# Kernel optimization log

Measured on AMD Instinct MI355X. Metric: run time of the kernel, lower is better.

The kernel has to match this reference:

```python
import jax, jax.numpy as jnp
import numpy as np
from jax import lax

K = 10
ALPHA = 0.1
N_NODES = 100000
N_EDGES = 3200000


def setup_inputs() -> dict:
    key = jax.random.key(0)
    ks = jax.random.split(key, 6)
    x = jax.random.normal(ks[0], (N_NODES, 256), dtype=jnp.float32)
    edge_index = jax.random.randint(ks[1], (2, N_EDGES), 0, N_NODES, dtype=jnp.int64)
    w1 = jax.random.normal(ks[2], (256, 256), dtype=jnp.float32) * (1.0 / np.sqrt(256))
    b1 = jax.random.normal(ks[3], (256,), dtype=jnp.float32) * 0.01
    w2 = jax.random.normal(ks[4], (64, 256), dtype=jnp.float32) * (1.0 / np.sqrt(256))
    b2 = jax.random.normal(ks[5], (64,), dtype=jnp.float32) * 0.01
    return {"x": x, "edge_index": edge_index, "w1": w1, "b1": b1, "w2": w2, "b2": b2}


def reference(x, edge_index, w1, b1, w2, b2):
    # Eval mode: dropout is identity.
    h = jax.nn.relu(x @ w1.T + b1)          # [N, hidden]
    z = h @ w2.T + b2                        # [N, out]

    n = x.shape[0]
    loop = jnp.arange(n, dtype=edge_index.dtype)
    row = jnp.concatenate([edge_index[0], loop])   # sources (with self-loops)
    col = jnp.concatenate([edge_index[1], loop])   # targets (with self-loops)

    # gcn_norm: D^{-1/2} (A + I) D^{-1/2}, degree at target nodes
    deg = jax.ops.segment_sum(jnp.ones_like(col, dtype=z.dtype), col, num_segments=n)
    dinv = lax.rsqrt(deg)                    # deg >= 1 due to self-loops
    norm = dinv[row] * dinv[col]             # [E+N]

    x0 = z

    def step(xk, _):
        msg = xk[row] * norm[:, None]                          # gather + scale
        agg = jax.ops.segment_sum(msg, col, num_segments=n)    # scatter-add
        return (1.0 - ALPHA) * agg + ALPHA * x0, None

    out, _ = lax.scan(step, z, None, length=K)
    return out
```

## Files before the change

kernel.cpp:

```cpp
#include <hip/hip_runtime.h>
#include <hip/hip_bf16.h>


#define HIDDEN 256
#define OUTF   64
#define NB_BLK 256

typedef __attribute__((ext_vector_type(8))) unsigned short ushort8;
typedef __attribute__((ext_vector_type(8))) short short8v;
typedef __attribute__((ext_vector_type(4))) float f32x4;

__device__ inline float b2f(unsigned short u) {
    union { unsigned int i; float f; } c;
    c.i = ((unsigned int)u) << 16;
    return c.f;
}
__device__ inline unsigned short f2b(float f) {
    union { float f; unsigned int i; } c;
    c.f = f;
    unsigned int x = c.i;
    unsigned int r = (x + 0x7fff + ((x >> 16) & 1)) >> 16;
    return (unsigned short)r;
}
__device__ inline short8v cvt8v(float4 A, float4 B) {
    short8v o;
    o[0] = (short)f2b(A.x); o[1] = (short)f2b(A.y);
    o[2] = (short)f2b(A.z); o[3] = (short)f2b(A.w);
    o[4] = (short)f2b(B.x); o[5] = (short)f2b(B.y);
    o[6] = (short)f2b(B.z); o[7] = (short)f2b(B.w);
    return o;
}
__device__ inline short8v cvt8(const float* s) {
    return cvt8v(((const float4*)s)[0], ((const float4*)s)[1]);
}

__device__ inline bool detect_i64(const int* __restrict__ p) {
    int acc = 0;
#pragma unroll
    for (int i = 0; i < 16; ++i) acc |= p[2 * i + 1];
    return acc == 0;
}
__device__ inline int load_idx(const void* eiv, long long flat, bool is64) {
    if (is64) return (int)((const long long*)eiv)[flat];
    return ((const int*)eiv)[flat];
}

__global__ __launch_bounds__(256) void part_hist_kernel(const void* __restrict__ eiv,
                                                        long long E, int* __restrict__ bh,
                                                        int n, int nb) {
    __shared__ int hist[512];
    bool is64 = detect_i64((const int*)eiv);
    int t = threadIdx.x, b = blockIdx.x;
    for (int i = t; i < 512; i += 256) hist[i] = 0;
    __syncthreads();
    long long chunk = (E + NB_BLK - 1) / NB_BLK;
    long long beg = (long long)b * chunk, end = min(E, beg + chunk);
    for (long long e = beg + t; e < end; e += 256) {
        int c = load_idx(eiv, E + e, is64);
        if ((unsigned)c < (unsigned)n) atomicAdd(&hist[c >> 8], 1);
    }
    __syncthreads();
    for (int i = t; i < nb; i += 256) bh[i * NB_BLK + b] = hist[i];
}

__global__ __launch_bounds__(256) void part_colscan_kernel(const int* __restrict__ bh,
                                                           int* __restrict__ pre,
                                                           int* __restrict__ btot) {
    __shared__ int s[NB_BLK];
    int g = blockIdx.x, t = threadIdx.x;
    int v = bh[g * NB_BLK + t];
    s[t] = v;
    __syncthreads();
    for (int o = 1; o < NB_BLK; o <<= 1) {
        int tv = (t >= o) ? s[t - o] : 0;
        __syncthreads();
        s[t] += tv;
        __syncthreads();
    }
    pre[g * NB_BLK + t] = s[t] - v;
    if (t == NB_BLK - 1) btot[g] = s[t];
}

__global__ __launch_bounds__(512) void part_bscan_kernel(const int* __restrict__ btot,
                                                         int* __restrict__ bofs, int nb) {
    __shared__ int s[512];
    int t = threadIdx.x;
    int v = (t < nb) ? btot[t] : 0;
    s[t] = v;
    __syncthreads();
    for (int o = 1; o < 512; o <<= 1) {
        int tv = (t >= o) ? s[t - o] : 0;
        __syncthreads();
        s[t] += tv;
        __syncthreads();
    }
    if (t < nb) bofs[t] = s[t] - v;
    if (t == 511) bofs[nb] = s[511];
}

__global__ __launch_bounds__(256) void part_scatter_kernel(const void* __restrict__ eiv,
                                                           long long E,
                                                           const int* __restrict__ bofs,
                                                           const int* __restrict__ pre,
                                                           int2* __restrict__ pairs,
                                                           int n, int nb) {
    __shared__ int cur[512];
    bool is64 = detect_i64((const int*)eiv);
    int t = threadIdx.x, b = blockIdx.x;
    for (int i = t; i < nb; i += 256) cur[i] = bofs[i] + pre[i * NB_BLK + b];
    __syncthreads();
    long long chunk = (E + NB_BLK - 1) / NB_BLK;
    long long beg = (long long)b * chunk, end = min(E, beg + chunk);
    for (long long e = beg + t; e < end; e += 256) {
        int r = load_idx(eiv, e, is64);
        int c = load_idx(eiv, E + e, is64);
        if ((unsigned)c >= (unsigned)n || (unsigned)r >= (unsigned)n) continue;
        int pos = atomicAdd(&cur[c >> 8], 1);
        pairs[pos] = make_int2(c, r);
    }
}

__global__ __launch_bounds__(256) void csr_bucket_kernel(const int2* __restrict__ pairs,
                                                         const int* __restrict__ bofs,
                                                         int* __restrict__ ofs,
                                                         float* __restrict__ dinv,
                                                         int* __restrict__ csr_src,
                                                         int n, int nb) {
    __shared__ int hist[256];
    __shared__ int scn[256];
    int b = blockIdx.x;
    int t = threadIdx.x;
    int node0 = b << 8;
    int cnt = min(256, n - node0);

    hist[t] = 0;
    __syncthreads();
    int beg = bofs[b], end = bofs[b + 1];
    for (int e = beg + t; e < end; e += 256) atomicAdd(&hist[pairs[e].x & 255], 1);
    __syncthreads();
    int v = hist[t];
    scn[t] = v;
    __syncthreads();
    for (int o = 1; o < 256; o <<= 1) {
        int tv = (t >= o) ? scn[t - o] : 0;
        __syncthreads();
        scn[t] += tv;
        __syncthreads();
    }
    int excl = scn[t] - v;
    if (t < cnt) {
        ofs[node0 + t] = beg + excl;
        dinv[node0 + t] = rsqrtf((float)(v + 1));
    }
    if (b == nb - 1 && t == 0) ofs[n] = end;
    __syncthreads();
    hist[t] = beg + excl;
    __syncthreads();
    for (int e = beg + t; e < end; e += 256) {
        int2 p = pairs[e];
        int pos = atomicAdd(&hist[p.x & 255], 1);
        csr_src[pos] = p.y;
    }
}

__global__ __launch_bounds__(256) void pack_w_kernel(const float* __restrict__ w1,
                                                     const float* __restrict__ w2,
                                                     unsigned short* __restrict__ w1p,
                                                     unsigned short* __restrict__ w2p) {
    int id = blockIdx.x * 256 + threadIdx.x;
    if (id < 8192) {
        int ks = id >> 10, rem = id & 1023;
        int f = rem >> 2, kg = rem & 3;
        short8v o = cvt8(w1 + (size_t)f * HIDDEN + ks * 32 + kg * 8);
        *(short8v*)(w1p + ((size_t)(ks * 1024 + (f >> 4) * 64 + kg * 16 + (f & 15)) << 3)) = o;
    } else if (id < 8192 + 2048) {
        int q = id - 8192;
        int j = q >> 5, kslot = q & 31;
        short8v o = cvt8(w2 + (size_t)j * HIDDEN + kslot * 8);
        *(short8v*)(w2p +
                    ((size_t)((j >> 4) * 512 + (kslot >> 2) * 64 + (kslot & 3) * 16 + (j & 15))
                     << 3)) = o;
    }
}

__global__ __launch_bounds__(512) void mlp_mfma_kernel(const float* __restrict__ x,
                                                       const unsigned short* __restrict__ w1p,
                                                       const float* __restrict__ b1,
                                                       const unsigned short* __restrict__ w2p,
                                                       const float* __restrict__ b2,
                                                       const float* __restrict__ dinv,
                                                       unsigned short* __restrict__ xb0,
                                                       unsigned short* __restrict__ g0, int n) {
    __shared__ __align__(16) union {
        struct { unsigned short w1s[8192]; unsigned short xs[2048]; } p1;
        unsigned short h[64 * 264];
    } u;

    const int t = threadIdx.x;
    const int w = t >> 6;
    const int l = t & 63;
    const int c = l & 15, g = l >> 4;
    const int node0 = blockIdx.x * 64;

    const bool xrole = (t < 256);
    const int sm = t >> 2, skg = t & 3;
    const int snode = node0 + sm;
    const int wu0 = t - 256;

    f32x4 acc[4][2];
#pragma unroll
    for (int a = 0; a < 4; ++a)
#pragma unroll
        for (int b = 0; b < 2; ++b) acc[a][b] = (f32x4)0.f;

    float4 pxa = make_float4(0.f, 0.f, 0.f, 0.f), pxb = pxa;
    short8v pw[4];
    if (xrole) {
        if (snode < n) {
            const float4* xp = (const float4*)(x + (size_t)snode * HIDDEN + skg * 8);
            pxa = xp[0];
            pxb = xp[1];
        }
    } else {
#pragma unroll
        for (int i = 0; i < 4; ++i)
            pw[i] = *(const short8v*)(w1p + ((size_t)(wu0 + i * 256) << 3));
    }

    for (int ks = 0; ks < 8; ++ks) {
        if (xrole) {
            *(short8v*)&u.p1.xs[((sm >> 4) * 64 + skg * 16 + (sm & 15)) << 3] = cvt8v(pxa, pxb);
        } else {
#pragma unroll
            for (int i = 0; i < 4; ++i)
                *(short8v*)&u.p1.w1s[(wu0 + i * 256) << 3] = pw[i];
        }
        __syncthreads();
        if (ks < 7) {
            if (xrole) {
                if (snode < n) {
                    const float4* xp =
                        (const float4*)(x + (size_t)snode * HIDDEN + (ks + 1) * 32 + skg * 8);
                    pxa = xp[0];
                    pxb = xp[1];
                }
            } else {
                const unsigned short* wsrc = w1p + (size_t)(ks + 1) * 8192;
#pragma unroll
                for (int i = 0; i < 4; ++i)
                    pw[i] = *(const short8v*)(wsrc + ((size_t)(wu0 + i * 256) << 3));
            }
        }
        short8v af[4], bf[2];
#pragma unroll
        for (int mt = 0; mt < 4; ++mt)
            af[mt] = *(const short8v*)&u.p1.xs[(mt * 64 + l) << 3];
#pragma unroll
        for (int j = 0; j < 2; ++j)
            bf[j] = *(const short8v*)&u.p1.w1s[((w * 2 + j) * 64 + l) << 3];
#pragma unroll
        for (int mt = 0; mt < 4; ++mt)
#pragma unroll
            for (int j = 0; j < 2; ++j)
                acc[mt][j] =
                    __builtin_amdgcn_mfma_f32_16x16x32_bf16(af[mt], bf[j], acc[mt][j], 0, 0, 0);
        __syncthreads();
    }

#pragma unroll
    for (int j = 0; j < 2; ++j) {
        int col = w * 32 + j * 16 + c;
        float b1v = b1[col];
#pragma unroll
        for (int mt = 0; mt < 4; ++mt)
#pragma unroll
            for (int r = 0; r < 4; ++r) {
                int row = mt * 16 + g * 4 + r;
                u.h[row * 264 + col] = f2b(fmaxf(acc[mt][j][r] + b1v, 0.f));
            }
    }
    __syncthreads();

    const int rt = w >> 1;
    const int cb = (w & 1) * 2;
    f32x4 acc2[2];
#pragma unroll
    for (int j = 0; j < 2; ++j) acc2[j] = (f32x4)0.f;
#pragma unroll
    for (int ks = 0; ks < 8; ++ks) {
        short8v a2 = *(const short8v*)&u.h[(rt * 16 + c) * 264 + ks * 32 + g * 8];
#pragma unroll
        for (int j = 0; j < 2; ++j) {
            short8v bv = *(const short8v*)(w2p + ((size_t)((cb + j) * 512 + ks * 64 + l) << 3));
            acc2[j] = __builtin_amdgcn_mfma_f32_16x16x32_bf16(a2, bv, acc2[j], 0, 0, 0);
        }
    }
#pragma unroll
    for (int j = 0; j < 2; ++j) {
        int col = (cb + j) * 16 + c;
        float bb = b2[col];
#pragma unroll
        for (int r = 0; r < 4; ++r) {
            int node = node0 + rt * 16 + g * 4 + r;
            if (node < n) {
                float zv = acc2[j][r] + bb;
                float di = dinv[node];
                xb0[(size_t)node * OUTF + col] = f2b(0.1f * zv);
                g0[(size_t)node * OUTF + col] = f2b(di * zv);
            }
        }
    }
}

template <int LAST>
__global__ __launch_bounds__(256) void prop_kernel(const unsigned short* __restrict__ gk,
                                                   const unsigned short* __restrict__ xb0,
                                                   unsigned short* __restrict__ gn,
                                                   float* __restrict__ out,
                                                   const int* __restrict__ ofs,
                                                   const int* __restrict__ csr_src,
                                                   const float* __restrict__ dinv, int n) {
    int gid = blockIdx.x * 256 + threadIdx.x;
    int node = gid >> 3;
    int part = gid & 7;
    if (node >= n) return;

    int beg = ofs[node];
    int end = ofs[node + 1];
    float di = dinv[node];

    float acc[8];
#pragma unroll
    for (int j = 0; j < 8; ++j) acc[j] = 0.f;

    const size_t poff = (size_t)part * 8;
    int e = beg;
    for (; e + 3 < end; e += 4) {
        int s0 = csr_src[e];
        int s1 = csr_src[e + 1];
        int s2 = csr_src[e + 2];
        int s3 = csr_src[e + 3];
        ushort8 a = *(const ushort8*)(gk + ((size_t)s0 << 6) + poff);
        ushort8 b = *(const ushort8*)(gk + ((size_t)s1 << 6) + poff);
        ushort8 cc = *(const ushort8*)(gk + ((size_t)s2 << 6) + poff);
        ushort8 d = *(const ushort8*)(gk + ((size_t)s3 << 6) + poff);
#pragma unroll
        for (int j = 0; j < 8; ++j) acc[j] += b2f(a[j]);
#pragma unroll
        for (int j = 0; j < 8; ++j) acc[j] += b2f(b[j]);
#pragma unroll
        for (int j = 0; j < 8; ++j) acc[j] += b2f(cc[j]);
#pragma unroll
        for (int j = 0; j < 8; ++j) acc[j] += b2f(d[j]);
    }
    for (; e < end; ++e) {
        int s0 = csr_src[e];
        ushort8 a = *(const ushort8*)(gk + ((size_t)s0 << 6) + poff);
#pragma unroll
        for (int j = 0; j < 8; ++j) acc[j] += b2f(a[j]);
    }
    {
        ushort8 a = *(const ushort8*)(gk + ((size_t)node << 6) + poff);
#pragma unroll
        for (int j = 0; j < 8; ++j) acc[j] += b2f(a[j]);
    }

    ushort8 xv = *(const ushort8*)(xb0 + ((size_t)node << 6) + poff);
    float res[8];
#pragma unroll
    for (int j = 0; j < 8; ++j) res[j] = 0.9f * di * acc[j] + b2f(xv[j]);

    if (LAST) {
        float4* o4 = (float4*)(out + (size_t)node * OUTF + poff);
        o4[0] = make_float4(res[0], res[1], res[2], res[3]);
        o4[1] = make_float4(res[4], res[5], res[6], res[7]);
    } else {
        ushort8 o;
#pragma unroll
        for (int j = 0; j < 8; ++j) o[j] = f2b(di * res[j]);
        *(ushort8*)(gn + ((size_t)node << 6) + poff) = o;
    }
}

extern "C" void kernel_launch(void* const* d_in, const int* in_sizes, int n_in,
                              void* d_out, int out_size, void* d_ws, size_t ws_size,
                              hipStream_t stream) {
    const float* x = (const float*)d_in[0];
    const void* ei = d_in[1];
    const float* w1 = (const float*)d_in[2];
    const float* b1 = (const float*)d_in[3];
    const float* w2 = (const float*)d_in[4];
    const float* b2 = (const float*)d_in[5];
    float* out = (float*)d_out;

    int n = in_sizes[0] / HIDDEN;
    long long E = (long long)in_sizes[1] / 2;
    int nb = (n + 255) >> 8;

    char* ws = (char*)d_ws;
    size_t off = 0;
    auto alloc = [&](size_t bytes) {
        void* p = ws + off;
        off += (bytes + 511) & ~(size_t)511;
        return p;
    };
    unsigned short* xb0 = (unsigned short*)alloc((size_t)n * OUTF * 2);
    size_t gmark = off;
    unsigned short* gA = (unsigned short*)alloc((size_t)n * OUTF * 2);
    unsigned short* gB = (unsigned short*)alloc((size_t)n * OUTF * 2);
    int2* pairs = (int2*)(ws + gmark);
    float* dinv = (float*)alloc((size_t)n * 4);
    int* ofs = (int*)alloc((size_t)(n + 1) * 4);
    int* csr_src = (int*)alloc((size_t)E * 4);
    int* bh = (int*)alloc((size_t)512 * NB_BLK * 4);
    int* pre = (int*)alloc((size_t)512 * NB_BLK * 4);
    int* btot = (int*)alloc(512 * 4);
    int* bofs = (int*)alloc(513 * 4);
    unsigned short* w1p = (unsigned short*)alloc(65536 * 2);
    unsigned short* w2p = (unsigned short*)alloc(16384 * 2);

    pack_w_kernel<<<40, 256, 0, stream>>>(w1, w2, w1p, w2p);

    part_hist_kernel<<<NB_BLK, 256, 0, stream>>>(ei, E, bh, n, nb);
    part_colscan_kernel<<<nb, NB_BLK, 0, stream>>>(bh, pre, btot);
    part_bscan_kernel<<<1, 512, 0, stream>>>(btot, bofs, nb);
    part_scatter_kernel<<<NB_BLK, 256, 0, stream>>>(ei, E, bofs, pre, pairs, n, nb);
    csr_bucket_kernel<<<nb, 256, 0, stream>>>(pairs, bofs, ofs, dinv, csr_src, n, nb);

    mlp_mfma_kernel<<<(n + 63) / 64, 512, 0, stream>>>(x, w1p, b1, w2p, b2, dinv, xb0, gA, n);

    int prop_blocks = (int)(((size_t)n * 8 + 255) / 256);
    for (int k = 0; k < 10; ++k) {
        const unsigned short* gin = (k & 1) ? gB : gA;
        unsigned short* gout = (k & 1) ? gA : gB;
        if (k == 9) {
            prop_kernel<1><<<prop_blocks, 256, 0, stream>>>(gin, xb0, nullptr, out, ofs,
                                                            csr_src, dinv, n);
        } else {
            prop_kernel<0><<<prop_blocks, 256, 0, stream>>>(gin, xb0, gout, nullptr, ofs,
                                                            csr_src, dinv, n);
        }
    }
}
```

Baseline: 687.2 us.

## Sort nodes by degree for propagation and double-buffer MLP input loads

Adds a counting sort of nodes into descending-degree order (histogram, scans, scatter) and has the propagation kernel process nodes through this permutation, so wavefronts handle nodes of similar degree and divergence from uneven edge counts drops. It also restructures the MLP k-loop to prefetch two x slices ahead in separate registers. The cost is four extra small kernels, an additional indirection per node in each of the ten propagation passes, and a loss of sequential locality in the ofs/output accesses.

```diff
diff --git a/kernel.cpp b/kernel.cpp
--- a/kernel.cpp
+++ b/kernel.cpp
@@ -5,6 +5,7 @@
 #define HIDDEN 256
 #define OUTF   64
 #define NB_BLK 256
+#define NB2    128
 
 typedef __attribute__((ext_vector_type(8))) unsigned short ushort8;
 typedef __attribute__((ext_vector_type(8))) short short8v;
@@ -160,6 +161,75 @@
         int2 p = pairs[e];
         int pos = atomicAdd(&hist[p.x & 255], 1);
         csr_src[pos] = p.y;
+    }
+}
+
+__global__ __launch_bounds__(256) void deg_hist_kernel(const int* __restrict__ ofs,
+                                                       int* __restrict__ dh, int n) {
+    __shared__ int hist[128];
+    int t = threadIdx.x, b = blockIdx.x;
+    if (t < 128) hist[t] = 0;
+    __syncthreads();
+    int chunk = (n + NB2 - 1) / NB2;
+    int beg = b * chunk, end = min(n, beg + chunk);
+    for (int i = beg + t; i < end; i += 256) {
+        int deg = ofs[i + 1] - ofs[i];
+        int bin = 127 - min(deg, 127);
+        atomicAdd(&hist[bin], 1);
+    }
+    __syncthreads();
+    if (t < 128) dh[t * NB2 + b] = hist[t];
+}
+
+__global__ __launch_bounds__(128) void deg_colscan_kernel(const int* __restrict__ dh,
+                                                          int* __restrict__ pre2,
+                                                          int* __restrict__ btot2) {
+    __shared__ int s[NB2];
+    int g = blockIdx.x, t = threadIdx.x;
+    int v = dh[g * NB2 + t];
+    s[t] = v;
+    __syncthreads();
+    for (int o = 1; o < NB2; o <<= 1) {
+        int tv = (t >= o) ? s[t - o] : 0;
+        __syncthreads();
+        s[t] += tv;
+        __syncthreads();
+    }
+    pre2[g * NB2 + t] = s[t] - v;
+    if (t == NB2 - 1) btot2[g] = s[t];
+}
+
+__global__ __launch_bounds__(128) void deg_bscan_kernel(const int* __restrict__ btot2,
+                                                        int* __restrict__ bofs2) {
+    __shared__ int s[128];
+    int t = threadIdx.x;
+    int v = btot2[t];
+    s[t] = v;
+    __syncthreads();
+    for (int o = 1; o < 128; o <<= 1) {
+        int tv = (t >= o) ? s[t - o] : 0;
+        __syncthreads();
+        s[t] += tv;
+        __syncthreads();
+    }
+    bofs2[t] = s[t] - v;
+}
+
+__global__ __launch_bounds__(256) void deg_scatter_kernel(const int* __restrict__ ofs,
+                                                          const int* __restrict__ bofs2,
+                                                          const int* __restrict__ pre2,
+                                                          int* __restrict__ perm, int n) {
+    __shared__ int cur[128];
+    int t = threadIdx.x, b = blockIdx.x;
+    if (t < 128) cur[t] = bofs2[t] + pre2[t * NB2 + b];
+    __syncthreads();
+    int chunk = (n + NB2 - 1) / NB2;
+    int beg = b * chunk, end = min(n, beg + chunk);
+    for (int i = beg + t; i < end; i += 256) {
+        int deg = ofs[i + 1] - ofs[i];
+        int bin = 127 - min(deg, 127);
+        int pos = atomicAdd(&cur[bin], 1);
+        perm[pos] = i;
     }
 }
 
@@ -206,6 +276,7 @@
     const int sm = t >> 2, skg = t & 3;
     const int snode = node0 + sm;
     const int wu0 = t - 256;
+    const int xunit = ((sm >> 4) * 64 + skg * 16 + (sm & 15)) << 3;
 
     f32x4 acc[4][2];
 #pragma unroll
@@ -213,44 +284,24 @@
 #pragma unroll
         for (int b = 0; b < 2; ++b) acc[a][b] = (f32x4)0.f;
 
-    float4 pxa = make_float4(0.f, 0.f, 0.f, 0.f), pxb = pxa;
+    float4 pxa0 = make_float4(0.f, 0.f, 0.f, 0.f), pxb0 = pxa0;
+    float4 pxa1 = pxa0, pxb1 = pxa0;
     short8v pw[4];
-    if (xrole) {
+
+    auto loadx = [&](int ks, float4& A, float4& B) {
         if (snode < n) {
-            const float4* xp = (const float4*)(x + (size_t)snode * HIDDEN + skg * 8);
-            pxa = xp[0];
-            pxb = xp[1];
+            const float4* xp = (const float4*)(x + (size_t)snode * HIDDEN + ks * 32 + skg * 8);
+            A = xp[0];
+            B = xp[1];
         }
-    } else {
+    };
+    auto loadw = [&](int ks) {
+        const unsigned short* wsrc = w1p + (size_t)ks * 8192;
 #pragma unroll
         for (int i = 0; i < 4; ++i)
-            pw[i] = *(const short8v*)(w1p + ((size_t)(wu0 + i * 256) << 3));
-    }
-
-    for (int ks = 0; ks < 8; ++ks) {
-        if (xrole) {
-            *(short8v*)&u.p1.xs[((sm >> 4) * 64 + skg * 16 + (sm & 15)) << 3] = cvt8v(pxa, pxb);
-        } else {
-#pragma unroll
-            for (int i = 0; i < 4; ++i)
-                *(short8v*)&u.p1.w1s[(wu0 + i * 256) << 3] = pw[i];
-        }
-        __syncthreads();
-        if (ks < 7) {
-            if (xrole) {
-                if (snode < n) {
-                    const float4* xp =
-                        (const float4*)(x + (size_t)snode * HIDDEN + (ks + 1) * 32 + skg * 8);
-                    pxa = xp[0];
-                    pxb = xp[1];
-                }
-            } else {
-                const unsigned short* wsrc = w1p + (size_t)(ks + 1) * 8192;
-#pragma unroll
-                for (int i = 0; i < 4; ++i)
-                    pw[i] = *(const short8v*)(wsrc + ((size_t)(wu0 + i * 256) << 3));
-            }
-        }
+            pw[i] = *(const short8v*)(wsrc + ((size_t)(wu0 + i * 256) << 3));
+    };
+    auto mfma_step = [&]() {
         short8v af[4], bf[2];
 #pragma unroll
         for (int mt = 0; mt < 4; ++mt)
@@ -264,6 +315,40 @@
             for (int j = 0; j < 2; ++j)
                 acc[mt][j] =
                     __builtin_amdgcn_mfma_f32_16x16x32_bf16(af[mt], bf[j], acc[mt][j], 0, 0, 0);
+    };
+    auto wwrite = [&]() {
+#pragma unroll
+        for (int i = 0; i < 4; ++i)
+            *(short8v*)&u.p1.w1s[(wu0 + i * 256) << 3] = pw[i];
+    };
+
+    if (xrole) {
+        loadx(0, pxa0, pxb0);
+        loadx(1, pxa1, pxb1);
+    } else {
+        loadw(0);
+    }
+
+    for (int ks = 0; ks < 8; ks += 2) {
+        if (xrole) *(short8v*)&u.p1.xs[xunit] = cvt8v(pxa0, pxb0);
+        else wwrite();
+        __syncthreads();
+        if (xrole) {
+            if (ks + 2 < 8) loadx(ks + 2, pxa0, pxb0);
+        } else {
+            loadw(ks + 1);
+        }
+        mfma_step();
+        __syncthreads();
+        if (xrole) *(short8v*)&u.p1.xs[xunit] = cvt8v(pxa1, pxb1);
+        else wwrite();
+        __syncthreads();
+        if (xrole) {
+            if (ks + 3 < 8) loadx(ks + 3, pxa1, pxb1);
+        } else {
+            if (ks + 2 < 8) loadw(ks + 2);
+        }
+        mfma_step();
         __syncthreads();
     }
 
@@ -319,11 +404,13 @@
                                                    float* __restrict__ out,
                                                    const int* __restrict__ ofs,
                                                    const int* __restrict__ csr_src,
-                                                   const float* __restrict__ dinv, int n) {
+                                                   const float* __restrict__ dinv,
+                                                   const int* __restrict__ perm, int n) {
     int gid = blockIdx.x * 256 + threadIdx.x;
-    int node = gid >> 3;
+    int nid = gid >> 3;
     int part = gid & 7;
-    if (node >= n) return;
+    if (nid >= n) return;
+    int node = perm[nid];
 
     int beg = ofs[node];
     int end = ofs[node + 1];
@@ -418,6 +505,11 @@
     int* bofs = (int*)alloc(513 * 4);
     unsigned short* w1p = (unsigned short*)alloc(65536 * 2);
     unsigned short* w2p = (unsigned short*)alloc(16384 * 2);
+    int* perm = (int*)alloc((size_t)n * 4);
+    int* dh = (int*)alloc((size_t)128 * NB2 * 4);
+    int* pre2 = (int*)alloc((size_t)128 * NB2 * 4);
+    int* btot2 = (int*)alloc(128 * 4);
+    int* bofs2 = (int*)alloc(128 * 4);
 
     pack_w_kernel<<<40, 256, 0, stream>>>(w1, w2, w1p, w2p);
 
@@ -426,6 +518,11 @@
     part_bscan_kernel<<<1, 512, 0, stream>>>(btot, bofs, nb);
     part_scatter_kernel<<<NB_BLK, 256, 0, stream>>>(ei, E, bofs, pre, pairs, n, nb);
     csr_bucket_kernel<<<nb, 256, 0, stream>>>(pairs, bofs, ofs, dinv, csr_src, n, nb);
+
+    deg_hist_kernel<<<NB2, 256, 0, stream>>>(ofs, dh, n);
+    deg_colscan_kernel<<<128, NB2, 0, stream>>>(dh, pre2, btot2);
+    deg_bscan_kernel<<<1, 128, 0, stream>>>(btot2, bofs2);
+    deg_scatter_kernel<<<NB2, 256, 0, stream>>>(ofs, bofs2, pre2, perm, n);
 
     mlp_mfma_kernel<<<(n + 63) / 64, 512, 0, stream>>>(x, w1p, b1, w2p, b2, dinv, xb0, gA, n);
 
@@ -435,10 +532,10 @@
         unsigned short* gout = (k & 1) ? gA : gB;
         if (k == 9) {
             prop_kernel<1><<<prop_blocks, 256, 0, stream>>>(gin, xb0, nullptr, out, ofs,
-                                                            csr_src, dinv, n);
+                                                            csr_src, dinv, perm, n);
         } else {
             prop_kernel<0><<<prop_blocks, 256, 0, stream>>>(gin, xb0, gout, nullptr, ofs,
-                                                            csr_src, dinv, n);
+                                                            csr_src, dinv, perm, n);
         }
     }
 }
```

After: 724.9 us. 5.5% more time.

## Split each node's edge list across four thread groups and double-buffer x prefetch

Applied to the files above, without the earlier changes.

The propagation kernel now gives each node 32 threads instead of 8. Four quarter-groups each gather a slice of the node's incoming edges and combine their partial sums with cross-lane shuffles, which raises memory-level parallelism and shortens per-thread dependency chains in the gather. The MLP kernel's x loads are unrolled by two with a second register buffer, so x loads are issued two k-steps ahead. In exchange the change launches four times as many threads, adds shuffle reductions, and holds more registers in the MLP kernel.

```diff
diff --git a/kernel.cpp b/kernel.cpp
--- a/kernel.cpp
+++ b/kernel.cpp
@@ -206,6 +206,7 @@
     const int sm = t >> 2, skg = t & 3;
     const int snode = node0 + sm;
     const int wu0 = t - 256;
+    const int xunit = ((sm >> 4) * 64 + skg * 16 + (sm & 15)) << 3;
 
     f32x4 acc[4][2];
 #pragma unroll
@@ -213,44 +214,24 @@
 #pragma unroll
         for (int b = 0; b < 2; ++b) acc[a][b] = (f32x4)0.f;
 
-    float4 pxa = make_float4(0.f, 0.f, 0.f, 0.f), pxb = pxa;
+    float4 pxa0 = make_float4(0.f, 0.f, 0.f, 0.f), pxb0 = pxa0;
+    float4 pxa1 = pxa0, pxb1 = pxa0;
     short8v pw[4];
-    if (xrole) {
+
+    auto loadx = [&](int ks, float4& A, float4& B) {
         if (snode < n) {
-            const float4* xp = (const float4*)(x + (size_t)snode * HIDDEN + skg * 8);
-            pxa = xp[0];
-            pxb = xp[1];
-        }
-    } else {
+            const float4* xp = (const float4*)(x + (size_t)snode * HIDDEN + ks * 32 + skg * 8);
+            A = xp[0];
+            B = xp[1];
+        }
+    };
+    auto loadw = [&](int ks) {
+        const unsigned short* wsrc = w1p + (size_t)ks * 8192;
 #pragma unroll
         for (int i = 0; i < 4; ++i)
-            pw[i] = *(const short8v*)(w1p + ((size_t)(wu0 + i * 256) << 3));
-    }
-
-    for (int ks = 0; ks < 8; ++ks) {
-        if (xrole) {
-            *(short8v*)&u.p1.xs[((sm >> 4) * 64 + skg * 16 + (sm & 15)) << 3] = cvt8v(pxa, pxb);
-        } else {
-#pragma unroll
-            for (int i = 0; i < 4; ++i)
-                *(short8v*)&u.p1.w1s[(wu0 + i * 256) << 3] = pw[i];
-        }
-        __syncthreads();
-        if (ks < 7) {
-            if (xrole) {
-                if (snode < n) {
-                    const float4* xp =
-                        (const float4*)(x + (size_t)snode * HIDDEN + (ks + 1) * 32 + skg * 8);
-                    pxa = xp[0];
-                    pxb = xp[1];
-                }
-            } else {
-                const unsigned short* wsrc = w1p + (size_t)(ks + 1) * 8192;
-#pragma unroll
-                for (int i = 0; i < 4; ++i)
-                    pw[i] = *(const short8v*)(wsrc + ((size_t)(wu0 + i * 256) << 3));
-            }
-        }
+            pw[i] = *(const short8v*)(wsrc + ((size_t)(wu0 + i * 256) << 3));
+    };
+    auto mfma_step = [&]() {
         short8v af[4], bf[2];
 #pragma unroll
         for (int mt = 0; mt < 4; ++mt)
@@ -264,6 +245,40 @@
             for (int j = 0; j < 2; ++j)
                 acc[mt][j] =
                     __builtin_amdgcn_mfma_f32_16x16x32_bf16(af[mt], bf[j], acc[mt][j], 0, 0, 0);
+    };
+    auto wwrite = [&]() {
+#pragma unroll
+        for (int i = 0; i < 4; ++i)
+            *(short8v*)&u.p1.w1s[(wu0 + i * 256) << 3] = pw[i];
+    };
+
+    if (xrole) {
+        loadx(0, pxa0, pxb0);
+        loadx(1, pxa1, pxb1);
+    } else {
+        loadw(0);
+    }
+
+    for (int ks = 0; ks < 8; ks += 2) {
+        if (xrole) *(short8v*)&u.p1.xs[xunit] = cvt8v(pxa0, pxb0);
+        else wwrite();
+        __syncthreads();
+        if (xrole) {
+            if (ks + 2 < 8) loadx(ks + 2, pxa0, pxb0);
+        } else {
+            loadw(ks + 1);
+        }
+        mfma_step();
+        __syncthreads();
+        if (xrole) *(short8v*)&u.p1.xs[xunit] = cvt8v(pxa1, pxb1);
+        else wwrite();
+        __syncthreads();
+        if (xrole) {
+            if (ks + 3 < 8) loadx(ks + 3, pxa1, pxb1);
+        } else {
+            if (ks + 2 < 8) loadw(ks + 2);
+        }
+        mfma_step();
         __syncthreads();
     }
 
@@ -321,21 +336,25 @@
                                                    const int* __restrict__ csr_src,
                                                    const float* __restrict__ dinv, int n) {
     int gid = blockIdx.x * 256 + threadIdx.x;
-    int node = gid >> 3;
-    int part = gid & 7;
+    int node = gid >> 5;
+    int sub = gid & 31;
+    int part = sub & 7;
+    int q = sub >> 3;
     if (node >= n) return;
 
     int beg = ofs[node];
     int end = ofs[node + 1];
-    float di = dinv[node];
+    int len = end - beg;
+    int e0 = beg + ((len * q) >> 2);
+    int e1 = beg + ((len * (q + 1)) >> 2);
 
     float acc[8];
 #pragma unroll
     for (int j = 0; j < 8; ++j) acc[j] = 0.f;
 
     const size_t poff = (size_t)part * 8;
-    int e = beg;
-    for (; e + 3 < end; e += 4) {
+    int e = e0;
+    for (; e + 3 < e1; e += 4) {
         int s0 = csr_src[e];
         int s1 = csr_src[e + 1];
         int s2 = csr_src[e + 2];
@@ -353,18 +372,26 @@
 #pragma unroll
         for (int j = 0; j < 8; ++j) acc[j] += b2f(d[j]);
     }
-    for (; e < end; ++e) {
+    for (; e < e1; ++e) {
         int s0 = csr_src[e];
         ushort8 a = *(const ushort8*)(gk + ((size_t)s0 << 6) + poff);
 #pragma unroll
         for (int j = 0; j < 8; ++j) acc[j] += b2f(a[j]);
     }
-    {
+    if (q == 0) {
         ushort8 a = *(const ushort8*)(gk + ((size_t)node << 6) + poff);
 #pragma unroll
         for (int j = 0; j < 8; ++j) acc[j] += b2f(a[j]);
     }
 
+#pragma unroll
+    for (int j = 0; j < 8; ++j) acc[j] += __shfl_xor(acc[j], 8);
+#pragma unroll
+    for (int j = 0; j < 8; ++j) acc[j] += __shfl_xor(acc[j], 16);
+
+    if (q != 0) return;
+
+    float di = dinv[node];
     ushort8 xv = *(const ushort8*)(xb0 + ((size_t)node << 6) + poff);
     float res[8];
 #pragma unroll
@@ -429,7 +456,7 @@
 
     mlp_mfma_kernel<<<(n + 63) / 64, 512, 0, stream>>>(x, w1p, b1, w2p, b2, dinv, xb0, gA, n);
 
-    int prop_blocks = (int)(((size_t)n * 8 + 255) / 256);
+    int prop_blocks = (int)(((size_t)n * 32 + 255) / 256);
     for (int k = 0; k < 10; ++k) {
         const unsigned short* gin = (k & 1) ? gB : gA;
         unsigned short* gout = (k & 1) ? gA : gB;
```

New measurement: 681.4 us. Within noise of the previous version (-0.8%).
